# Performance work log

Measured on AMD Instinct MI355X. Metric: run time of the kernel, lower is better.

## Reference

```python
import jax, jax.numpy as jnp
import numpy as np

B, S, D, H = 2, 2048, 1024, 16
DK = D // H


def setup_inputs() -> dict:
    key = jax.random.key(0)
    ks = jax.random.split(key, 7)
    q = jax.random.normal(ks[0], (B, S, D), dtype=jnp.float32)
    k = jax.random.normal(ks[1], (B, S, D), dtype=jnp.float32)
    v = jax.random.normal(ks[2], (B, S, D), dtype=jnp.float32)
    # causal mask (1 = keep, 0 = mask) broadcast over batch/heads
    mask = jnp.tril(jnp.ones((S, S), dtype=jnp.int32))[None, None, :, :]
    scale = 1.0 / np.sqrt(DK)
    W_q = jax.random.normal(ks[3], (D, D), dtype=jnp.float32) * 0.02
    W_k = jax.random.normal(ks[4], (D, D), dtype=jnp.float32) * 0.02
    W_v = jax.random.normal(ks[5], (D, D), dtype=jnp.float32) * 0.02
    W_o = jax.random.normal(ks[6], (D, D), dtype=jnp.float32) * 0.02
    return {"q": q, "k": k, "v": v, "mask": mask,
            "W_q": W_q, "W_k": W_k, "W_v": W_v, "W_o": W_o}


def _split_heads(x):
    # [B, S, D] -> [B, H, S, DK]
    b, s, _ = x.shape
    return x.reshape(b, s, H, DK).transpose(0, 2, 1, 3)


def reference(q, k, v, mask, W_q, W_k, W_v, W_o):
    # nn.Linear(bias=False): y = x @ W.T
    qh = _split_heads(q @ W_q.T)
    kh = _split_heads(k @ W_k.T)
    vh = _split_heads(v @ W_v.T)
    scores = jnp.einsum("bhqd,bhkd->bhqk", qh, kh) / np.sqrt(DK)
    scores = jnp.where(mask == 0, jnp.float32(-1e9), scores)
    attn = jax.nn.softmax(scores, axis=-1)  # dropout p=0 -> identity
    out = jnp.einsum("bhqk,bhkd->bhqd", attn, vh)
    out = out.transpose(0, 2, 1, 3).reshape(q.shape[0], q.shape[1], D)
    return out @ W_o.T
```

## Files before the change

### kernel.cpp

```cpp
#include <hip/hip_runtime.h>
#include <stdint.h>
#include <stddef.h>

typedef __bf16 bf16;
typedef __attribute__((ext_vector_type(4))) __bf16 bf16x4;
typedef __attribute__((ext_vector_type(8))) __bf16 bf16x8;
typedef __attribute__((ext_vector_type(4))) float floatx4;

#define NB 2
#define NS 2048
#define ND 1024
#define NH 16
#define NDK 64
#define NBH (NB*NH)
#define NBS (NB*NS)

__device__ inline void gl2lds16(const bf16* g, bf16* l) {
  __builtin_amdgcn_global_load_lds(
      (const __attribute__((address_space(1))) uint32_t*)(const uint32_t*)(g),
      (__attribute__((address_space(3))) uint32_t*)(uint32_t*)(l),
      16, 0, 0);
}

__global__ __launch_bounds__(256)
void convert_w(const float* __restrict__ Wq, const float* __restrict__ Wk,
               const float* __restrict__ Wv, bf16* __restrict__ Wb)
{
  const int z = blockIdx.y;
  const float* src = (z == 0) ? Wq : (z == 1) ? Wk : Wv;
  bf16* dst = Wb + (size_t)z * (ND * ND);
  const size_t off = ((size_t)blockIdx.x * 256 + threadIdx.x) * 32;
#pragma unroll
  for (int c = 0; c < 2; c++) {
    bf16x8 o[2];
#pragma unroll
    for (int h = 0; h < 2; h++) {
      const float4 a = *(const float4*)(src + off + c * 16 + h * 8);
      const float4 b = *(const float4*)(src + off + c * 16 + h * 8 + 4);
      o[h][0] = (bf16)a.x; o[h][1] = (bf16)a.y; o[h][2] = (bf16)a.z; o[h][3] = (bf16)a.w;
      o[h][4] = (bf16)b.x; o[h][5] = (bf16)b.y; o[h][6] = (bf16)b.z; o[h][7] = (bf16)b.w;
    }
    *(bf16x8*)(dst + off + c * 16) = o[0];
    *(bf16x8*)(dst + off + c * 16 + 8) = o[1];
  }
}

__global__ __launch_bounds__(256)
void proj_gemm(const float* __restrict__ q, const float* __restrict__ k,
               const float* __restrict__ v, const bf16* __restrict__ Wb,
               bf16* __restrict__ Qh, bf16* __restrict__ Kh,
               bf16* __restrict__ Vt)
{
  const int z = blockIdx.y, bx = blockIdx.x;
  const int tid = threadIdx.x;
  const int wave = tid >> 6, lane = tid & 63;
  const int quad = lane >> 4, l15 = lane & 15;

  const float* X = (z == 0) ? q : (z == 1) ? k : v;
  const bf16* W = Wb + (size_t)z * (ND * ND);
  const int c = bx & 7, r = bx >> 3;
  const int m0 = (c * 4 + (r >> 3)) * 128, n0 = (r & 7) * 128;

  __shared__ bf16 As[2][128 * 32];
  __shared__ bf16 Bs[2][128 * 32];

  const int arow = tid >> 3, ach = tid & 7;
  const int brow = tid >> 2, bch = tid & 3;

  floatx4 acc[4][4];
#pragma unroll
  for (int i = 0; i < 4; i++)
#pragma unroll
    for (int j = 0; j < 4; j++) acc[i][j] = (floatx4)(0.0f);

  const int wm = (wave >> 1) * 64, wn = (wave & 1) * 64;

  float4 ra[4];
#pragma unroll
  for (int it = 0; it < 4; it++)
    ra[it] = *(const float4*)(X + (size_t)(m0 + it * 32 + arow) * ND + ach * 4);
#pragma unroll
  for (int it = 0; it < 2; it++)
    gl2lds16(W + (size_t)(n0 + it * 64 + brow) * ND + bch * 8,
             Bs[0] + (it * 256 + tid) * 8);
  __builtin_amdgcn_s_waitcnt(0);
#pragma unroll
  for (int it = 0; it < 4; it++) {
    bf16x4 a;
    a[0] = (bf16)ra[it].x; a[1] = (bf16)ra[it].y;
    a[2] = (bf16)ra[it].z; a[3] = (bf16)ra[it].w;
    *(bf16x4*)(As[0] + (it * 32 + arow) * 32 + ach * 4) = a;
  }
#pragma unroll
  for (int it = 0; it < 4; it++)
    ra[it] = *(const float4*)(X + (size_t)(m0 + it * 32 + arow) * ND + 32 + ach * 4);

  for (int kk = 0; kk < 32; kk++) {
    const int cur = kk & 1, nxt = cur ^ 1;
    __builtin_amdgcn_s_waitcnt(0);
    __syncthreads();
    if (kk + 1 < 32) {
      const int k1 = (kk + 1) * 32;
#pragma unroll
      for (int it = 0; it < 2; it++)
        gl2lds16(W + (size_t)(n0 + it * 64 + brow) * ND + k1 + bch * 8,
                 Bs[nxt] + (it * 256 + tid) * 8);
#pragma unroll
      for (int it = 0; it < 4; it++) {
        bf16x4 a;
        a[0] = (bf16)ra[it].x; a[1] = (bf16)ra[it].y;
        a[2] = (bf16)ra[it].z; a[3] = (bf16)ra[it].w;
        *(bf16x4*)(As[nxt] + (it * 32 + arow) * 32 + ach * 4) = a;
      }
      if (kk + 2 < 32) {
        const int k2 = (kk + 2) * 32;
#pragma unroll
        for (int it = 0; it < 4; it++)
          ra[it] = *(const float4*)(X + (size_t)(m0 + it * 32 + arow) * ND + k2 + ach * 4);
      }
    }
    bf16x8 af[4], bfr[4];
#pragma unroll
    for (int i = 0; i < 4; i++)
      af[i] = *(const bf16x8*)(As[cur] + (wm + i * 16 + l15) * 32 + quad * 8);
#pragma unroll
    for (int j = 0; j < 4; j++)
      bfr[j] = *(const bf16x8*)(Bs[cur] + (wn + j * 16 + l15) * 32 + quad * 8);
#pragma unroll
    for (int i = 0; i < 4; i++)
#pragma unroll
      for (int j = 0; j < 4; j++)
        acc[i][j] = __builtin_amdgcn_mfma_f32_16x16x32_bf16(af[i], bfr[j],
                                                            acc[i][j], 0, 0, 0);
  }

  bf16* O = (z == 0) ? Qh : (z == 1) ? Kh : Vt;
#pragma unroll
  for (int i = 0; i < 4; i++) {
    const int rowb = m0 + wm + i * 16 + quad * 4;
#pragma unroll
    for (int j = 0; j < 4; j++) {
      const int col = n0 + wn + j * 16 + l15;
#pragma unroll
      for (int rr = 0; rr < 4; rr++) {
        const int row = rowb + rr;
        const bf16 o = (bf16)acc[i][j][rr];
        const int b = row >> 11, s = row & 2047;
        const int h = col >> 6,  dk = col & 63;
        if (z < 2)
          O[(((size_t)(b * NH + h)) * NS + s) * NDK + dk] = o;
        else
          O[(((size_t)(b * NH + h)) * NDK + dk) * NS + s] = o;
      }
    }
  }
}

__global__ __launch_bounds__(256)
void attn_fwd(const bf16* __restrict__ Qh, const bf16* __restrict__ Kh,
              const bf16* __restrict__ Vt, bf16* __restrict__ Ctx)
{
  const int x = blockIdx.x, bh = blockIdx.y;
  const int tid = threadIdx.x, wave = tid >> 6, lane = tid & 63;
  const int quad = lane >> 4, l15 = lane & 15;

  __shared__ bf16 Ks[2][64 * 64];
  __shared__ bf16 Vs[2][64 * 64];
  __shared__ bf16 Ps[4][16 * 64];

  const size_t qkb = (size_t)bh * NS * NDK;
  const size_t vb  = (size_t)bh * NDK * NS;
  const int b = bh >> 4, h = bh & 15;
  const float C = 0.125f * 1.44269504088896f;

  auto stage = [&](int kt, int buf) {
#pragma unroll
    for (int it = 0; it < 2; it++) {
      const int lin = it * 256 + tid;
      const int row = lin >> 3;
      const int chS = (lin & 7) ^ (row & 7);
      gl2lds16(Kh + qkb + (size_t)(kt * 64 + row) * NDK + chS * 8,
               Ks[buf] + lin * 8);
      gl2lds16(Vt + vb + (size_t)row * NS + kt * 64 + chS * 8,
               Vs[buf] + lin * 8);
    }
  };

  for (int ph = 0; ph < 2; ph++) {
    const int qt = ph ? x : 31 - x;
    const int qrow0 = qt * 64 + wave * 16;

    bf16x8 qf0, qf1;
    {
      const bf16* qp = Qh + qkb + (size_t)(qrow0 + l15) * NDK + quad * 8;
      qf0 = *(const bf16x8*)qp;
      qf1 = *(const bf16x8*)(qp + 32);
    }

    float lsum[4] = {0.0f, 0.0f, 0.0f, 0.0f};
    floatx4 oacc[4];
#pragma unroll
    for (int j = 0; j < 4; j++) oacc[j] = (floatx4)(0.0f);

    __syncthreads();
    stage(0, 0);

    for (int kt = 0; kt <= qt; kt++) {
      const int cur = kt & 1;
      __builtin_amdgcn_s_waitcnt(0);
      __syncthreads();
      if (kt < qt) stage(kt + 1, cur ^ 1);

      const bf16* Ksb = Ks[cur];
      const bf16* Vsb = Vs[cur];

      floatx4 sa[4];
#pragma unroll
      for (int jt = 0; jt < 4; jt++) {
        const int rr = jt * 16 + l15;
        const bf16x8 kf0 = *(const bf16x8*)(Ksb + rr * 64 + ((quad ^ (rr & 7)) << 3));
        const bf16x8 kf1 = *(const bf16x8*)(Ksb + rr * 64 + (((4 + quad) ^ (rr & 7)) << 3));
        floatx4 zz = (floatx4)(0.0f);
        zz = __builtin_amdgcn_mfma_f32_16x16x32_bf16(qf0, kf0, zz, 0, 0, 0);
        zz = __builtin_amdgcn_mfma_f32_16x16x32_bf16(qf1, kf1, zz, 0, 0, 0);
        sa[jt] = zz;
      }

      const bool diag = (kt == qt);
#pragma unroll
      for (int jt = 0; jt < 4; jt++) {
        const int col = jt * 16 + l15;
#pragma unroll
        for (int rr = 0; rr < 4; rr++) {
          const int row = quad * 4 + rr;
          float p = exp2f(sa[jt][rr] * C);
          if (diag) p = (kt * 64 + col <= qrow0 + row) ? p : 0.0f;
          lsum[rr] += p;
          Ps[wave][row * 64 + ((((col >> 3) ^ (row & 7))) << 3) + (col & 7)] =
              (bf16)p;
        }
      }

#pragma unroll
      for (int ks = 0; ks < 2; ks++) {
        const bf16x8 pf = *(const bf16x8*)(
            &Ps[wave][l15 * 64 + (((ks * 4 + quad) ^ (l15 & 7)) << 3)]);
#pragma unroll
        for (int jt = 0; jt < 4; jt++) {
          const int rr = jt * 16 + l15;
          const bf16x8 vf = *(const bf16x8*)(
              Vsb + rr * 64 + (((ks * 4 + quad) ^ (rr & 7)) << 3));
          oacc[jt] = __builtin_amdgcn_mfma_f32_16x16x32_bf16(pf, vf,
                                                             oacc[jt], 0, 0, 0);
        }
      }
    }

#pragma unroll
    for (int off = 1; off < 16; off <<= 1)
#pragma unroll
      for (int rr = 0; rr < 4; rr++) lsum[rr] += __shfl_xor(lsum[rr], off, 64);

#pragma unroll
    for (int jt = 0; jt < 4; jt++)
#pragma unroll
      for (int rr = 0; rr < 4; rr++) {
        const int srow = qrow0 + quad * 4 + rr;
        Ctx[((size_t)b * NS + srow) * ND + h * 64 + jt * 16 + l15] =
            (bf16)(oacc[jt][rr] / lsum[rr]);
      }
  }
}

__global__ __launch_bounds__(256)
void out_gemm(const bf16* __restrict__ Ctx, const float* __restrict__ Wo,
              float* __restrict__ out)
{
  const int bx = blockIdx.x, tid = threadIdx.x;
  const int wave = tid >> 6, lane = tid & 63;
  const int quad = lane >> 4, l15 = lane & 15;
  const int c = bx & 7, r = bx >> 3;
  const int m0 = (c * 8 + (r >> 3)) * 64, n0 = (r & 7) * 128;
  const int wm = (wave & 1) * 32, wn = (wave >> 1) * 64;

  __shared__ bf16 As[2][64 * 32];
  __shared__ bf16 Bs[2][128 * 32];

  const int arow = tid >> 2, ach = tid & 3;
  const int brow = tid >> 3, bch = tid & 7;

  floatx4 acc[2][4];
#pragma unroll
  for (int i = 0; i < 2; i++)
#pragma unroll
    for (int j = 0; j < 4; j++) acc[i][j] = (floatx4)(0.0f);

  float4 rb[4];
  gl2lds16(Ctx + (size_t)(m0 + arow) * ND + ach * 8, As[0] + tid * 8);
#pragma unroll
  for (int it = 0; it < 4; it++)
    rb[it] = *(const float4*)(Wo + (size_t)(n0 + it * 32 + brow) * ND + bch * 4);
  __builtin_amdgcn_s_waitcnt(0);
#pragma unroll
  for (int it = 0; it < 4; it++) {
    bf16x4 bb;
    bb[0] = (bf16)rb[it].x; bb[1] = (bf16)rb[it].y;
    bb[2] = (bf16)rb[it].z; bb[3] = (bf16)rb[it].w;
    *(bf16x4*)(Bs[0] + (it * 32 + brow) * 32 + bch * 4) = bb;
  }
#pragma unroll
  for (int it = 0; it < 4; it++)
    rb[it] = *(const float4*)(Wo + (size_t)(n0 + it * 32 + brow) * ND + 32 + bch * 4);

  for (int kk = 0; kk < 32; kk++) {
    const int cur = kk & 1, nxt = cur ^ 1;
    __builtin_amdgcn_s_waitcnt(0);
    __syncthreads();
    if (kk + 1 < 32) {
      const int k1 = (kk + 1) * 32;
      gl2lds16(Ctx + (size_t)(m0 + arow) * ND + k1 + ach * 8, As[nxt] + tid * 8);
#pragma unroll
      for (int it = 0; it < 4; it++) {
        bf16x4 bb;
        bb[0] = (bf16)rb[it].x; bb[1] = (bf16)rb[it].y;
        bb[2] = (bf16)rb[it].z; bb[3] = (bf16)rb[it].w;
        *(bf16x4*)(Bs[nxt] + (it * 32 + brow) * 32 + bch * 4) = bb;
      }
      if (kk + 2 < 32) {
        const int k2 = (kk + 2) * 32;
#pragma unroll
        for (int it = 0; it < 4; it++)
          rb[it] = *(const float4*)(Wo + (size_t)(n0 + it * 32 + brow) * ND + k2 + bch * 4);
      }
    }
    bf16x8 af[2], bfr[4];
#pragma unroll
    for (int i = 0; i < 2; i++)
      af[i] = *(const bf16x8*)(As[cur] + (wm + i * 16 + l15) * 32 + quad * 8);
#pragma unroll
    for (int j = 0; j < 4; j++)
      bfr[j] = *(const bf16x8*)(Bs[cur] + (wn + j * 16 + l15) * 32 + quad * 8);
#pragma unroll
    for (int i = 0; i < 2; i++)
#pragma unroll
      for (int j = 0; j < 4; j++)
        acc[i][j] = __builtin_amdgcn_mfma_f32_16x16x32_bf16(af[i], bfr[j],
                                                            acc[i][j], 0, 0, 0);
  }

#pragma unroll
  for (int i = 0; i < 2; i++) {
    const int rowb = m0 + wm + i * 16 + quad * 4;
#pragma unroll
    for (int j = 0; j < 4; j++) {
      const int col = n0 + wn + j * 16 + l15;
#pragma unroll
      for (int rr = 0; rr < 4; rr++)
        out[(size_t)(rowb + rr) * ND + col] = acc[i][j][rr];
    }
  }
}

extern "C" void kernel_launch(void* const* d_in, const int* in_sizes, int n_in,
                              void* d_out, int out_size, void* d_ws, size_t ws_size,
                              hipStream_t stream) {
  const float* q  = (const float*)d_in[0];
  const float* k  = (const float*)d_in[1];
  const float* v  = (const float*)d_in[2];
  const float* Wq = (const float*)d_in[4];
  const float* Wk = (const float*)d_in[5];
  const float* Wv = (const float*)d_in[6];
  const float* Wo = (const float*)d_in[7];
  float* out = (float*)d_out;

  const size_t elems = (size_t)NBS * ND;
  bf16* Qh  = (bf16*)d_ws;
  bf16* Kh  = Qh + elems;
  bf16* Vt  = Kh + elems;
  bf16* Ctx = Vt + elems;
  bf16* Wb  = Ctx;

  dim3 blk(256);
  convert_w<<<dim3(128, 3), blk, 0, stream>>>(Wq, Wk, Wv, Wb);
  proj_gemm<<<dim3(256, 3), blk, 0, stream>>>(q, k, v, Wb, Qh, Kh, Vt);
  attn_fwd<<<dim3(16, NBH), blk, 0, stream>>>(Qh, Kh, Vt, Ctx);
  out_gemm<<<dim3(512), blk, 0, stream>>>(Ctx, Wo, out);
}
```

Baseline: 275.8 us.

## Stage fp32 activations via direct global-to-LDS loads and pre-convert Wo to bf16

The projection GEMM now copies fp32 activation tiles straight into LDS with global_load_lds, using an XOR-swizzled layout. The bf16 conversion moves to the fragment read from LDS, which removes the register-staged prefetch and the conversion stores. Wo is converted to bf16 by a separate small kernel into the free Vt workspace after attention, so out_gemm loads both operands with direct LDS copies. In exchange, proj_gemm uses twice the LDS for the A tile (possibly lower occupancy), the load-to-LDS path now has only single-stage overlap, and there is one extra kernel launch.

```diff
diff --git a/kernel.cpp b/kernel.cpp
--- a/kernel.cpp
+++ b/kernel.cpp
@@ -15,16 +15,16 @@
 #define NBH (NB*NH)
 #define NBS (NB*NS)
 
-__device__ inline void gl2lds16(const bf16* g, bf16* l) {
+__device__ inline void gl2lds16(const void* g, void* l) {
   __builtin_amdgcn_global_load_lds(
-      (const __attribute__((address_space(1))) uint32_t*)(const uint32_t*)(g),
-      (__attribute__((address_space(3))) uint32_t*)(uint32_t*)(l),
+      (const __attribute__((address_space(1))) uint32_t*)(const uint32_t*)g,
+      (__attribute__((address_space(3))) uint32_t*)(uint32_t*)l,
       16, 0, 0);
 }
 
 __global__ __launch_bounds__(256)
-void convert_w(const float* __restrict__ Wq, const float* __restrict__ Wk,
-               const float* __restrict__ Wv, bf16* __restrict__ Wb)
+void convert_w3(const float* __restrict__ Wq, const float* __restrict__ Wk,
+                const float* __restrict__ Wv, bf16* __restrict__ Wb)
 {
   const int z = blockIdx.y;
   const float* src = (z == 0) ? Wq : (z == 1) ? Wk : Wv;
@@ -46,6 +46,25 @@
 }
 
 __global__ __launch_bounds__(256)
+void convert_w1(const float* __restrict__ src, bf16* __restrict__ dst)
+{
+  const size_t off = ((size_t)blockIdx.x * 256 + threadIdx.x) * 32;
+#pragma unroll
+  for (int c = 0; c < 2; c++) {
+    bf16x8 o[2];
+#pragma unroll
+    for (int h = 0; h < 2; h++) {
+      const float4 a = *(const float4*)(src + off + c * 16 + h * 8);
+      const float4 b = *(const float4*)(src + off + c * 16 + h * 8 + 4);
+      o[h][0] = (bf16)a.x; o[h][1] = (bf16)a.y; o[h][2] = (bf16)a.z; o[h][3] = (bf16)a.w;
+      o[h][4] = (bf16)b.x; o[h][5] = (bf16)b.y; o[h][6] = (bf16)b.z; o[h][7] = (bf16)b.w;
+    }
+    *(bf16x8*)(dst + off + c * 16) = o[0];
+    *(bf16x8*)(dst + off + c * 16 + 8) = o[1];
+  }
+}
+
+__global__ __launch_bounds__(256)
 void proj_gemm(const float* __restrict__ q, const float* __restrict__ k,
                const float* __restrict__ v, const bf16* __restrict__ Wb,
                bf16* __restrict__ Qh, bf16* __restrict__ Kh,
@@ -61,11 +80,10 @@
   const int c = bx & 7, r = bx >> 3;
   const int m0 = (c * 4 + (r >> 3)) * 128, n0 = (r & 7) * 128;
 
-  __shared__ bf16 As[2][128 * 32];
-  __shared__ bf16 Bs[2][128 * 32];
-
-  const int arow = tid >> 3, ach = tid & 7;
-  const int brow = tid >> 2, bch = tid & 3;
+  __shared__ float Af[2][128 * 32];
+  __shared__ bf16  Bs[2][128 * 32];
+
+  const int wm = (wave >> 1) * 64, wn = (wave & 1) * 64;
 
   floatx4 acc[4][4];
 #pragma unroll
@@ -73,56 +91,44 @@
 #pragma unroll
     for (int j = 0; j < 4; j++) acc[i][j] = (floatx4)(0.0f);
 
-  const int wm = (wave >> 1) * 64, wn = (wave & 1) * 64;
-
-  float4 ra[4];
-#pragma unroll
-  for (int it = 0; it < 4; it++)
-    ra[it] = *(const float4*)(X + (size_t)(m0 + it * 32 + arow) * ND + ach * 4);
-#pragma unroll
-  for (int it = 0; it < 2; it++)
-    gl2lds16(W + (size_t)(n0 + it * 64 + brow) * ND + bch * 8,
-             Bs[0] + (it * 256 + tid) * 8);
-  __builtin_amdgcn_s_waitcnt(0);
-#pragma unroll
-  for (int it = 0; it < 4; it++) {
-    bf16x4 a;
-    a[0] = (bf16)ra[it].x; a[1] = (bf16)ra[it].y;
-    a[2] = (bf16)ra[it].z; a[3] = (bf16)ra[it].w;
-    *(bf16x4*)(As[0] + (it * 32 + arow) * 32 + ach * 4) = a;
-  }
-#pragma unroll
-  for (int it = 0; it < 4; it++)
-    ra[it] = *(const float4*)(X + (size_t)(m0 + it * 32 + arow) * ND + 32 + ach * 4);
-
+  auto stage = [&](int kt, int buf) {
+    const int k0 = kt * 32;
+#pragma unroll
+    for (int it = 0; it < 4; it++) {
+      const int lin = it * 256 + tid;
+      const int row = lin >> 3, slot = lin & 7;
+      const int srcCh = slot ^ (row & 7);
+      gl2lds16(X + (size_t)(m0 + row) * ND + k0 + srcCh * 4,
+               Af[buf] + row * 32 + slot * 4);
+    }
+#pragma unroll
+    for (int it = 0; it < 2; it++) {
+      const int lin = it * 256 + tid;
+      const int row = lin >> 2, ch = lin & 3;
+      gl2lds16(W + (size_t)(n0 + row) * ND + k0 + ch * 8,
+               Bs[buf] + lin * 8);
+    }
+  };
+
+  stage(0, 0);
   for (int kk = 0; kk < 32; kk++) {
-    const int cur = kk & 1, nxt = cur ^ 1;
+    const int cur = kk & 1;
     __builtin_amdgcn_s_waitcnt(0);
     __syncthreads();
-    if (kk + 1 < 32) {
-      const int k1 = (kk + 1) * 32;
-#pragma unroll
-      for (int it = 0; it < 2; it++)
-        gl2lds16(W + (size_t)(n0 + it * 64 + brow) * ND + k1 + bch * 8,
-                 Bs[nxt] + (it * 256 + tid) * 8);
-#pragma unroll
-      for (int it = 0; it < 4; it++) {
-        bf16x4 a;
-        a[0] = (bf16)ra[it].x; a[1] = (bf16)ra[it].y;
-        a[2] = (bf16)ra[it].z; a[3] = (bf16)ra[it].w;
-        *(bf16x4*)(As[nxt] + (it * 32 + arow) * 32 + ach * 4) = a;
-      }
-      if (kk + 2 < 32) {
-        const int k2 = (kk + 2) * 32;
-#pragma unroll
-        for (int it = 0; it < 4; it++)
-          ra[it] = *(const float4*)(X + (size_t)(m0 + it * 32 + arow) * ND + k2 + ach * 4);
-      }
-    }
+    if (kk + 1 < 32) stage(kk + 1, cur ^ 1);
+
     bf16x8 af[4], bfr[4];
 #pragma unroll
-    for (int i = 0; i < 4; i++)
-      af[i] = *(const bf16x8*)(As[cur] + (wm + i * 16 + l15) * 32 + quad * 8);
+    for (int i = 0; i < 4; i++) {
+      const int rl = wm + i * 16 + l15, r7 = rl & 7;
+      const float* Ab = Af[cur] + rl * 32;
+      const float4 p0 = *(const float4*)(Ab + (((2 * quad) ^ r7) << 2));
+      const float4 p1 = *(const float4*)(Ab + (((2 * quad + 1) ^ r7) << 2));
+      bf16x8 a;
+      a[0] = (bf16)p0.x; a[1] = (bf16)p0.y; a[2] = (bf16)p0.z; a[3] = (bf16)p0.w;
+      a[4] = (bf16)p1.x; a[5] = (bf16)p1.y; a[6] = (bf16)p1.z; a[7] = (bf16)p1.w;
+      af[i] = a;
+    }
 #pragma unroll
     for (int j = 0; j < 4; j++)
       bfr[j] = *(const bf16x8*)(Bs[cur] + (wn + j * 16 + l15) * 32 + quad * 8);
@@ -273,7 +279,7 @@
 }
 
 __global__ __launch_bounds__(256)
-void out_gemm(const bf16* __restrict__ Ctx, const float* __restrict__ Wo,
+void out_gemm(const bf16* __restrict__ Ctx, const bf16* __restrict__ WoB,
               float* __restrict__ out)
 {
   const int bx = blockIdx.x, tid = threadIdx.x;
@@ -286,53 +292,33 @@
   __shared__ bf16 As[2][64 * 32];
   __shared__ bf16 Bs[2][128 * 32];
 
-  const int arow = tid >> 2, ach = tid & 3;
-  const int brow = tid >> 3, bch = tid & 7;
-
   floatx4 acc[2][4];
 #pragma unroll
   for (int i = 0; i < 2; i++)
 #pragma unroll
     for (int j = 0; j < 4; j++) acc[i][j] = (floatx4)(0.0f);
 
-  float4 rb[4];
-  gl2lds16(Ctx + (size_t)(m0 + arow) * ND + ach * 8, As[0] + tid * 8);
-#pragma unroll
-  for (int it = 0; it < 4; it++)
-    rb[it] = *(const float4*)(Wo + (size_t)(n0 + it * 32 + brow) * ND + bch * 4);
-  __builtin_amdgcn_s_waitcnt(0);
-#pragma unroll
-  for (int it = 0; it < 4; it++) {
-    bf16x4 bb;
-    bb[0] = (bf16)rb[it].x; bb[1] = (bf16)rb[it].y;
-    bb[2] = (bf16)rb[it].z; bb[3] = (bf16)rb[it].w;
-    *(bf16x4*)(Bs[0] + (it * 32 + brow) * 32 + bch * 4) = bb;
-  }
-#pragma unroll
-  for (int it = 0; it < 4; it++)
-    rb[it] = *(const float4*)(Wo + (size_t)(n0 + it * 32 + brow) * ND + 32 + bch * 4);
-
+  auto stage = [&](int kt, int buf) {
+    const int k0 = kt * 32;
+    {
+      const int row = tid >> 2, ch = tid & 3;
+      gl2lds16(Ctx + (size_t)(m0 + row) * ND + k0 + ch * 8, As[buf] + tid * 8);
+    }
+#pragma unroll
+    for (int it = 0; it < 2; it++) {
+      const int lin = it * 256 + tid;
+      const int row = lin >> 2, ch = lin & 3;
+      gl2lds16(WoB + (size_t)(n0 + row) * ND + k0 + ch * 8, Bs[buf] + lin * 8);
+    }
+  };
+
+  stage(0, 0);
   for (int kk = 0; kk < 32; kk++) {
-    const int cur = kk & 1, nxt = cur ^ 1;
+    const int cur = kk & 1;
     __builtin_amdgcn_s_waitcnt(0);
     __syncthreads();
-    if (kk + 1 < 32) {
-      const int k1 = (kk + 1) * 32;
-      gl2lds16(Ctx + (size_t)(m0 + arow) * ND + k1 + ach * 8, As[nxt] + tid * 8);
-#pragma unroll
-      for (int it = 0; it < 4; it++) {
-        bf16x4 bb;
-        bb[0] = (bf16)rb[it].x; bb[1] = (bf16)rb[it].y;
-        bb[2] = (bf16)rb[it].z; bb[3] = (bf16)rb[it].w;
-        *(bf16x4*)(Bs[nxt] + (it * 32 + brow) * 32 + bch * 4) = bb;
-      }
-      if (kk + 2 < 32) {
-        const int k2 = (kk + 2) * 32;
-#pragma unroll
-        for (int it = 0; it < 4; it++)
-          rb[it] = *(const float4*)(Wo + (size_t)(n0 + it * 32 + brow) * ND + k2 + bch * 4);
-      }
-    }
+    if (kk + 1 < 32) stage(kk + 1, cur ^ 1);
+
     bf16x8 af[2], bfr[4];
 #pragma unroll
     for (int i = 0; i < 2; i++)
@@ -379,10 +365,12 @@
   bf16* Vt  = Kh + elems;
   bf16* Ctx = Vt + elems;
   bf16* Wb  = Ctx;
+  bf16* WoB = Vt;
 
   dim3 blk(256);
-  convert_w<<<dim3(128, 3), blk, 0, stream>>>(Wq, Wk, Wv, Wb);
+  convert_w3<<<dim3(128, 3), blk, 0, stream>>>(Wq, Wk, Wv, Wb);
   proj_gemm<<<dim3(256, 3), blk, 0, stream>>>(q, k, v, Wb, Qh, Kh, Vt);
   attn_fwd<<<dim3(16, NBH), blk, 0, stream>>>(Qh, Kh, Vt, Ctx);
-  out_gemm<<<dim3(512), blk, 0, stream>>>(Ctx, Wo, out);
-}
+  convert_w1<<<dim3(128), blk, 0, stream>>>(Wo, WoB);
+  out_gemm<<<dim3(512), blk, 0, stream>>>(Ctx, WoB, out);
+}
```

Result: slower. 285.0 us (+3.4%).
